# Kernel tuning notes

Measured on AMD Instinct MI355X. Metric: run time of the kernel, lower is better.

## Reference

```python
import jax, jax.numpy as jnp
import numpy as np

B, L, H, V = 64, 2048, 512, 34
T = 600           # max_decode_length hard-coded in Speller.forward
SOS_TOKEN = 0


def setup_inputs() -> dict:
    key = jax.random.key(0)
    ks = jax.random.split(key, 16)
    s = 1.0 / np.sqrt(H)
    p = lambda k, shape: (jax.random.uniform(k, shape, jnp.float32) * 2 - 1) * s
    return {
        "seq_embeddings": jax.random.normal(ks[0], (B, L, H), jnp.float32),
        "seq_lengths": jnp.maximum(jax.random.randint(ks[1], (B,), 0, L + 1), 1),
        "E_char": jax.random.normal(ks[2], (V, H), jnp.float32),      # nn.Embedding
        "W_key": p(ks[3], (H, H)), "b_key": p(ks[4], (H,)),           # Attention key_mlp
        "W_val": p(ks[5], (H, H)), "b_val": p(ks[6], (H,)),           # Attention value_mlp
        "W_ih": p(ks[7], (4 * H, 2 * H)), "W_hh": p(ks[8], (4 * H, H)),  # LSTMCell
        "b_ih": p(ks[9], (4 * H,)), "b_hh": p(ks[10], (4 * H,)),
        "W_cdn": p(ks[11], (V, 2 * H)), "b_cdn": p(ks[12], (V,)),     # cdn linear
    }


def reference(seq_embeddings, seq_lengths, E_char, W_key, b_key, W_val, b_val,
              W_ih, W_hh, b_ih, b_hh, W_cdn, b_cdn):
    Bz, Lz, Hz = seq_embeddings.shape
    # keys/values are time-invariant; compute once (same math as per-step recompute)
    keys = jnp.einsum('blh,kh->blk', seq_embeddings, W_key) + b_key       # (B,L,H)
    values = jnp.einsum('blh,kh->blk', seq_embeddings, W_val) + b_val     # (B,L,H)
    mask = jnp.arange(Lz)[None, :] < seq_lengths[:, None]                 # (B,L) ragged
    scale = 1.0 / jnp.sqrt(jnp.asarray(Hz, seq_embeddings.dtype))

    def attend(q):  # q: (B,H) -> masked softmax attention context (B,H)
        scores = jnp.einsum('blk,bk->bl', keys, q) * scale
        scores = jnp.where(mask, scores, -jnp.inf)
        w = jax.nn.softmax(scores, axis=1)                                # zeros past length
        return jnp.einsum('bl,blk->bk', w, values)

    h0 = jnp.zeros((Bz, Hz), seq_embeddings.dtype)
    c0 = jnp.zeros_like(h0)
    ctx0 = attend(h0)  # initial context with zero query -> uniform over valid positions
    rng = jax.random.key(42)

    def step(carry, t):
        prev_y, h, c, ctx = carry
        x = jnp.concatenate([E_char[prev_y], ctx], axis=1)                # (B,2H)
        gates = x @ W_ih.T + b_ih + h @ W_hh.T + b_hh                     # (B,4H)
        i, f, g, o = jnp.split(gates, 4, axis=1)
        c = jax.nn.sigmoid(f) * c + jax.nn.sigmoid(i) * jnp.tanh(g)
        h = jax.nn.sigmoid(o) * jnp.tanh(c)
        ctx = attend(h)
        logits = jnp.concatenate([h, ctx], axis=1) @ W_cdn.T + b_cdn      # (B,V)
        y = jax.random.categorical(jax.random.fold_in(rng, t), logits, axis=-1)
        return (y, h, c, ctx), y

    prev_y0 = jnp.full((Bz,), SOS_TOKEN, jnp.int32)
    _, ys = jax.lax.scan(step, (prev_y0, h0, c0, ctx0), jnp.arange(T))
    return ys.T  # (B, T) sampled symbols
```

## Files before the change

kernel.cpp:

```cpp
#include <hip/hip_runtime.h>
#include <cstdint>
#include <cfloat>
#include <cmath>

#define NB 64
#define LL 2048
#define HH 512
#define VV 34
#define TT 600
#define BLKT 512
#define GRID 256
#define GBLK 32
#define BSTRIDE 544

#define PARTITIONABLE 1

#define LDC(p)    __hip_atomic_load((p), __ATOMIC_RELAXED, __HIP_MEMORY_SCOPE_AGENT)
#define STC(p,v)  __hip_atomic_store((p), (v), __ATOMIC_RELAXED, __HIP_MEMORY_SCOPE_AGENT)

__device__ __forceinline__ float sigm_(float x){ return 1.0f/(1.0f+expf(-x)); }
__device__ __forceinline__ unsigned rotl_(unsigned x, int r){ return (x<<r)|(x>>(32-r)); }

__device__ __forceinline__ void tf2x32_(unsigned k0, unsigned k1, unsigned x0, unsigned x1,
                                        unsigned &o0, unsigned &o1){
  unsigned ks2 = k0 ^ k1 ^ 0x1BD11BDAu;
  x0 += k0; x1 += k1;
  x0+=x1; x1=rotl_(x1,13); x1^=x0;
  x0+=x1; x1=rotl_(x1,15); x1^=x0;
  x0+=x1; x1=rotl_(x1,26); x1^=x0;
  x0+=x1; x1=rotl_(x1, 6); x1^=x0;
  x0+=k1; x1+=ks2+1u;
  x0+=x1; x1=rotl_(x1,17); x1^=x0;
  x0+=x1; x1=rotl_(x1,29); x1^=x0;
  x0+=x1; x1=rotl_(x1,16); x1^=x0;
  x0+=x1; x1=rotl_(x1,24); x1^=x0;
  x0+=ks2; x1+=k0+2u;
  x0+=x1; x1=rotl_(x1,13); x1^=x0;
  x0+=x1; x1=rotl_(x1,15); x1^=x0;
  x0+=x1; x1=rotl_(x1,26); x1^=x0;
  x0+=x1; x1=rotl_(x1, 6); x1^=x0;
  x0+=k0; x1+=k1+3u;
  x0+=x1; x1=rotl_(x1,17); x1^=x0;
  x0+=x1; x1=rotl_(x1,29); x1^=x0;
  x0+=x1; x1=rotl_(x1,16); x1^=x0;
  x0+=x1; x1=rotl_(x1,24); x1^=x0;
  x0+=k1; x1+=ks2+4u;
  x0+=x1; x1=rotl_(x1,13); x1^=x0;
  x0+=x1; x1=rotl_(x1,15); x1^=x0;
  x0+=x1; x1=rotl_(x1,26); x1^=x0;
  x0+=x1; x1=rotl_(x1, 6); x1^=x0;
  x0+=ks2; x1+=k0+5u;
  o0 = x0; o1 = x1;
}

__device__ __forceinline__ void gumbel_emit_(int tid, int bb, int t, float* sZ,
                                             int* yv, int* out){
  if (tid < 34){
    unsigned kk0, kk1; tf2x32_(0u, 42u, 0u, (unsigned)t, kk0, kk1);
    int idx = bb*34 + tid;
    unsigned o0, o1, bits;
#if PARTITIONABLE
    tf2x32_(kk0, kk1, 0u, (unsigned)idx, o0, o1);
    bits = o0 ^ o1;
#else
    if (idx < 1088){ tf2x32_(kk0, kk1, (unsigned)idx, (unsigned)(idx+1088), o0, o1); bits = o0; }
    else           { tf2x32_(kk0, kk1, (unsigned)(idx-1088), (unsigned)idx, o0, o1); bits = o1; }
#endif
    float f = __uint_as_float((bits>>9) | 0x3f800000u) - 1.0f;
    float u = fmaxf(f, 1.17549435e-38f);
    sZ[tid] += -logf(-logf(u));
  }
  __syncthreads();
  if (tid == 0){
    float best = sZ[0]; int bi = 0;
    for (int v2=1; v2<34; v2++){ if (sZ[v2] > best){ best = sZ[v2]; bi = v2; } }
    STC(&yv[bb], bi);
    STC(&out[bb*TT + t], bi);
  }
}

__global__ __launch_bounds__(BLKT, 2) void speller_kernel_g32(
    const float* __restrict__ seq, const int* __restrict__ slen,
    const float* __restrict__ Ech, const float* __restrict__ Wkey,
    const float* __restrict__ Wval, const float* __restrict__ bval,
    const float* __restrict__ Wih, const float* __restrict__ Whh,
    const float* __restrict__ bih, const float* __restrict__ bhh,
    const float* __restrict__ Wcdn, const float* __restrict__ bcdn,
    int* __restrict__ out, float* __restrict__ ws, int MS, int CH)
{
  const int tid = threadIdx.x;
  const int bid = blockIdx.x;
  const int grp = bid & 7;
  const int li  = bid >> 3;

  float* h0   = ws;
  float* h1   = h0 + NB*HH;
  float* qt   = h1 + NB*HH;
  float* ctx  = qt + NB*HH;
  float* pm   = ctx + NB*HH;
  float* ps   = pm + NB*MS;
  float* pacc = ps + NB*MS;
  int*   iw   = (int*)(pacc + (size_t)NB*MS*HH);
  int*   yv   = iw;
  int*   bar  = iw + 64;

  __shared__ float sX[24*516];
  __shared__ float sRed[8*8*64];
  __shared__ float sGate[512];
  __shared__ float sAcc[8*512];
  __shared__ float sQt[512];
  __shared__ float sHb[512];
  __shared__ float sWm[8], sWs[8], sWf[8];
  __shared__ float sEb[512], sHs[512], sCt[512];
  __shared__ float sP[34*8];
  __shared__ float sZ[34];
  __shared__ float sAm[32], sAs[32], sAf[32];
  __shared__ float sSc[2];
  __shared__ int   sYv[8], sLen[8], sPref[9], sMap[8];

  float creg = 0.f;
  int epoch = 0;

  auto gbar = [&](){
    __syncthreads();
    epoch++;
    if (tid == 0)
      STC(&bar[grp*BSTRIDE + li*16], epoch);
    if (li == 0){
      if (tid < 32){
        while (LDC(&bar[grp*BSTRIDE + tid*16]) < epoch)
          __builtin_amdgcn_s_sleep(1);
      }
      if (tid == 0)
        STC(&bar[grp*BSTRIDE + 512], epoch);
    } else {
      if (tid == 0){
        while (LDC(&bar[grp*BSTRIDE + 512]) < epoch)
          __builtin_amdgcn_s_sleep(1);
      }
    }
    __syncthreads();
  };

  if (tid == 0){
    int ln[64]; unsigned char used[64];
    int load[8], cnt[8];
    for (int i=0;i<64;i++){
      int l = slen[i]; if (l<1) l=1; if (l>LL) l=LL;
      ln[i] = l; used[i] = 0;
    }
    for (int g2=0; g2<8; g2++){ load[g2]=0; cnt[g2]=0; }
    for (int it=0; it<64; it++){
      int bi = -1, bl = -1;
      for (int i=0;i<64;i++) if (!used[i] && ln[i] > bl){ bl = ln[i]; bi = i; }
      used[bi] = 1;
      int gi = -1, gl = 0x7fffffff;
      for (int g2=0; g2<8; g2++) if (cnt[g2] < 8 && load[g2] < gl){ gl = load[g2]; gi = g2; }
      if (gi == grp) sMap[cnt[gi]] = bi;
      load[gi] += bl; cnt[gi]++;
    }
  }
  __syncthreads();

  if (li < 8){
    int bb = sMap[li];
    STC(&h0[(size_t)bb*HH + tid], 0.f);
    STC(&h1[(size_t)bb*HH + tid], 0.f);
    STC(&qt[(size_t)bb*HH + tid], 0.f);
  }
  if (li == 8 && tid < 8) STC(&yv[sMap[tid]], 0);


  auto phaseA = [&](const float* hr, float* hw){
    if (tid < 8) sYv[tid] = LDC(&yv[sMap[tid]]);
    __syncthreads();
    #pragma unroll
    for (int i = 0; i < 24; i++){
      int b = i & 7, s = i >> 3;
      int bb = sMap[b];
      float v;
      if (s == 0)      v = Ech[(size_t)sYv[b]*HH + tid];
      else if (s == 1) v = LDC(&ctx[(size_t)bb*HH + tid]);
      else             v = LDC(&hr[(size_t)bb*HH + tid]);
      sX[i*516 + tid] = v;
    }
    __syncthreads();
    const int w = tid >> 6, lane = tid & 63, rr = lane >> 3, bb = lane & 7;
    float acc[8];
    #pragma unroll
    for (int o=0;o<8;o++) acc[o]=0.f;
    for (int kt = 0; kt < 12; kt++){
      const int sec = (kt < 4) ? 0 : (kt < 8) ? 1 : 2;
      const int cb4 = (kt & 3) * 128;
      #pragma unroll
      for (int it = 0; it < 4; it++){
        int kkb = w*16 + it*4;
        const float* xp = &sX[(sec*8 + bb)*516 + cb4 + kkb];
        float x0 = xp[0], x1 = xp[1], x2 = xp[2], x3 = xp[3];
        #pragma unroll
        for (int o = 0; o < 8; o++){
          int jl = o*8 + rr;
          int j  = (jl >> 4)*512 + li*16 + (jl & 15);
          const float* wp = (kt < 8) ? Wih + (size_t)j*1024 + kt*128 + kkb
                                     : Whh + (size_t)j*512  + (kt-8)*128 + kkb;
          float4 wv = *(const float4*)wp;
          acc[o] += wv.x*x0; acc[o] += wv.y*x1;
          acc[o] += wv.z*x2; acc[o] += wv.w*x3;
        }
      }
    }
    __syncthreads();
    #pragma unroll
    for (int o=0;o<8;o++) sRed[(w*8+o)*64 + lane] = acc[o];
    __syncthreads();
    {
      int jl = tid >> 3, b2 = tid & 7;
      int o = jl >> 3, rr2 = jl & 7;
      int j = (jl >> 4)*512 + li*16 + (jl & 15);
      float g = bih[j] + bhh[j];
      #pragma unroll
      for (int w2 = 0; w2 < 8; w2++) g += sRed[(w2*8+o)*64 + rr2*8 + b2];
      sGate[jl*8 + b2] = g;
    }
    __syncthreads();
    if (tid < 128){
      int kp = tid >> 3, b3 = tid & 7;
      float gi = sGate[(0*16+kp)*8 + b3];
      float gf = sGate[(1*16+kp)*8 + b3];
      float gg = sGate[(2*16+kp)*8 + b3];
      float go = sGate[(3*16+kp)*8 + b3];
      float cn = sigm_(gf)*creg + sigm_(gi)*tanhf(gg);
      creg = cn;
      STC(&hw[(size_t)sMap[b3]*HH + li*16 + kp], sigm_(go)*tanhf(cn));
    }
  };

  auto phaseB = [&](const float* hw){
    const int cc = li & 7;
    const int bp = li >> 3;
    const int bb0 = sMap[2*bp], bb1 = sMap[2*bp+1];
    sHb[tid] = LDC(&hw[(size_t)bb0*HH + tid]);
    sQt[tid] = LDC(&hw[(size_t)bb1*HH + tid]);
    float a = 0.f;
    const int c  = tid & 63;
    const int bs = (tid >> 6) & 1;
    for (int tile = 0; tile < 4; tile++){
      const int k0 = tile * 128;
      __syncthreads();
      {
        const float4* src = (const float4*)(Wkey + (size_t)k0*HH + cc*64);
        float4* dst = (float4*)sX;
        #pragma unroll
        for (int r = 0; r < 4; r++){
          int idx = r*512 + tid;
          int kk = idx >> 4, c4 = idx & 15;
          dst[kk*16 + c4] = src[(size_t)kk*(HH/4) + c4];
        }
      }
      __syncthreads();
      if (tid < 128){
        const float* hv = bs ? sQt : sHb;
        for (int kk = 0; kk < 128; kk++)
          a += sX[kk*64 + c] * hv[k0 + kk];
      }
    }
    __syncthreads();
    if (tid < 128){
      int bbX = bs ? bb1 : bb0;
      STC(&qt[(size_t)bbX*HH + cc*64 + c], a);
    }
  };

  auto phaseC = [&](){
    if (tid < 8){ int l = slen[sMap[tid]]; if(l<1)l=1; if(l>LL)l=LL; sLen[tid]=l; }
    __syncthreads();
    if (tid == 0){
      sPref[0] = 0;
      for (int i=0;i<8;i++) sPref[i+1] = sPref[i] + (sLen[i]+CH-1)/CH;
    }
    __syncthreads();
    const int gTot = sPref[8];
    const int w = tid >> 6, lane = tid & 63;
    const float SCALE = 1.0f / sqrtf(512.0f);
    const int start = (li*gTot)/GBLK, end = ((li+1)*gTot)/GBLK;
    int b = 0, bLast = -1;
    for (int c = start; c < end; ++c){
      while (sPref[b+1] <= c) b++;
      int slot = c - sPref[b];
      int l0 = slot * CH;
      int lend = min(l0 + CH, sLen[b]);
      int bb = sMap[b];
      if (b != bLast){
        __syncthreads();
        sQt[tid] = LDC(&qt[(size_t)bb*HH + tid]);
        bLast = b;
      }
      __syncthreads();
      const float4* qp = (const float4*)sQt;
      float4 qa = qp[lane], qb = qp[64+lane];
      float m = -FLT_MAX, ss = 0.f;
      float4 aA = make_float4(0,0,0,0), aB = make_float4(0,0,0,0);
      for (int ls = l0; ls < lend; ls += 64){
        float4 ra[8], rb[8];
        #pragma unroll
        for (int d=0; d<8; d++){
          int row = ls + w + d*8;
          if (row < lend){
            const float4* rp = (const float4*)(seq + ((size_t)bb*LL + row)*HH);
            ra[d] = rp[lane]; rb[d] = rp[64+lane];
          }
        }
        #pragma unroll
        for (int d=0; d<8; d++){
          int row = ls + w + d*8;
          if (row < lend){
            float4 ea = ra[d], eb = rb[d];
            float dd = ea.x*qa.x + ea.y*qa.y + ea.z*qa.z + ea.w*qa.w
                     + eb.x*qb.x + eb.y*qb.y + eb.z*qb.z + eb.w*qb.w;
            #pragma unroll
            for (int msk=1; msk<64; msk<<=1) dd += __shfl_xor(dd, msk, 64);
            float sc = dd * SCALE;
            float mn = fmaxf(m, sc);
            float r1 = expf(m - mn);
            float w1 = expf(sc - mn);
            ss = ss*r1 + w1;
            aA.x = aA.x*r1 + w1*ea.x; aA.y = aA.y*r1 + w1*ea.y;
            aA.z = aA.z*r1 + w1*ea.z; aA.w = aA.w*r1 + w1*ea.w;
            aB.x = aB.x*r1 + w1*eb.x; aB.y = aB.y*r1 + w1*eb.y;
            aB.z = aB.z*r1 + w1*eb.z; aB.w = aB.w*r1 + w1*eb.w;
            m = mn;
          }
        }
      }
      ((float4*)(sAcc + w*512))[lane]    = aA;
      ((float4*)(sAcc + w*512))[64+lane] = aB;
      if (lane == 0){ sWm[w] = m; sWs[w] = ss; }
      __syncthreads();
      if (tid == 0){
        float M = sWm[0];
        #pragma unroll
        for (int i=1;i<8;i++) M = fmaxf(M, sWm[i]);
        float S = 0.f;
        #pragma unroll
        for (int i=0;i<8;i++){ float f = expf(sWm[i]-M); sWf[i]=f; S += sWs[i]*f; }
        STC(&pm[bb*MS+slot], M); STC(&ps[bb*MS+slot], S);
      }
      __syncthreads();
      {
        float v = 0.f;
        #pragma unroll
        for (int i=0;i<8;i++) v += sAcc[i*512 + tid] * sWf[i];
        STC(&pacc[((size_t)(bb*MS+slot))*HH + tid], v);
      }
    }
  };

  auto phaseD = [&](int t, const float* hw){
    if (li < 8){
      const int bb = sMap[li];
      int ln = slen[bb]; if(ln<1)ln=1; if(ln>LL)ln=LL;
      const int nsl = (ln + CH - 1)/CH;
      if (tid < nsl){ sAm[tid] = LDC(&pm[bb*MS + tid]); sAs[tid] = LDC(&ps[bb*MS + tid]); }
      __syncthreads();
      if (tid == 0){
        float M = sAm[0];
        for (int s=1;s<nsl;s++) M = fmaxf(M, sAm[s]);
        float S = 0.f;
        for (int s=0;s<nsl;s++){ float f = expf(sAm[s]-M); sAf[s] = f; S += sAs[s]*f; }
        sSc[0] = S;
      }
      __syncthreads();
      {
        float S = sSc[0];
        float v = 0.f;
        #pragma unroll 8
        for (int s=0;s<nsl;s++) v += LDC(&pacc[((size_t)(bb*MS+s))*HH + tid]) * sAf[s];
        sEb[tid] = v / S;
        sHs[tid] = LDC(&hw[(size_t)bb*HH + tid]);
      }
      __syncthreads();
      {
        const float4* wr = (const float4*)(Wval + (size_t)tid*HH);
        const float4* er = (const float4*)sEb;
        float a = bval[tid];
        #pragma unroll 8
        for (int i=0;i<HH/4;i++){
          float4 w4 = wr[i], e4 = er[i];
          a += w4.x*e4.x; a += w4.y*e4.y; a += w4.z*e4.z; a += w4.w*e4.w;
        }
        sCt[tid] = a;
        STC(&ctx[(size_t)bb*HH + tid], a);
      }
      __syncthreads();
      if (t >= 0){
        if (tid < 34*8){
          int v = tid >> 3, ks = tid & 7;
          const float* wr = Wcdn + (size_t)v*1024 + ks*128;
          const float* xr = (ks < 4) ? (sHs + ks*128) : (sCt + (ks-4)*128);
          float p = 0.f;
          #pragma unroll 8
          for (int i=0;i<128;i++) p += wr[i]*xr[i];
          sP[v*8+ks] = p;
        }
        __syncthreads();
        if (tid < 34){
          float lg = bcdn[tid];
          #pragma unroll
          for (int i=0;i<8;i++) lg += sP[tid*8+i];
          sZ[tid] = lg;
        }
        __syncthreads();
        gumbel_emit_(tid, bb, t, sZ, yv, out);
      }
    }
  };

  gbar();
  phaseC();
  gbar();
  phaseD(-1, h0);
  gbar();
  for (int t = 0; t < TT; t++){
    const float* hr = (t & 1) ? h1 : h0;
    float* hwv      = (t & 1) ? h0 : h1;
    phaseA(hr, hwv);
    gbar();
    phaseB(hwv);
    gbar();
    phaseC();
    gbar();
    phaseD(t, hwv);
    gbar();
  }
}

extern "C" void kernel_launch(void* const* d_in, const int* in_sizes, int n_in,
                              void* d_out, int out_size, void* d_ws, size_t ws_size,
                              hipStream_t stream)
{
  const float* seq  = (const float*)d_in[0];
  const int*   slen = (const int*)d_in[1];
  const float* Ech  = (const float*)d_in[2];
  const float* Wkey = (const float*)d_in[3];
  const float* Wval = (const float*)d_in[5];
  const float* bval = (const float*)d_in[6];
  const float* Wih  = (const float*)d_in[7];
  const float* Whh  = (const float*)d_in[8];
  const float* bih  = (const float*)d_in[9];
  const float* bhh  = (const float*)d_in[10];
  const float* Wcdn = (const float*)d_in[11];
  const float* bcdn = (const float*)d_in[12];
  int*   out = (int*)d_out;
  float* ws  = (float*)d_ws;

  int MS = 32;
  size_t floats_total;
  while (true){
    floats_total = 4*(size_t)NB*HH + (size_t)NB*MS*(2 + HH);
    size_t need = (floats_total + 64 + 8*BSTRIDE + 64)*4;
    if (need <= ws_size || MS == 1) break;
    MS >>= 1;
  }
  int CH = 2048 / MS;

  size_t bar_off = (floats_total + 64)*4;
  hipMemsetAsync((char*)d_ws + bar_off, 0, 8*BSTRIDE*4, stream);

  void* args[] = { (void*)&seq, (void*)&slen, (void*)&Ech, (void*)&Wkey,
                   (void*)&Wval, (void*)&bval, (void*)&Wih, (void*)&Whh,
                   (void*)&bih, (void*)&bhh, (void*)&Wcdn, (void*)&bcdn,
                   (void*)&out, (void*)&ws, (void*)&MS, (void*)&CH };

  hipLaunchCooperativeKernel((void*)speller_kernel_g32, dim3(GRID), dim3(BLKT),
                             args, 0, stream);
}
```

Measured before the change: 71.00 ms.

## Split context phase across all group blocks and flatten group barrier

The per-batch context phase, previously run by only 8 of 32 blocks per group, is split into three phases. These are the softmax-combine, the Wval projection and the logits/sampling step, and the first two are spread over all 32 blocks by column quarters, reusing the stale h buffer as scratch for the normalized context. The group barrier is also flattened so every block polls all 32 block flags directly instead of going through a leader block. This trades more parallelism per phase for two extra grid barriers per decode step and more polling traffic.

```diff
diff --git a/kernel.cpp b/kernel.cpp
--- a/kernel.cpp
+++ b/kernel.cpp
@@ -126,18 +126,9 @@
     epoch++;
     if (tid == 0)
       STC(&bar[grp*BSTRIDE + li*16], epoch);
-    if (li == 0){
-      if (tid < 32){
-        while (LDC(&bar[grp*BSTRIDE + tid*16]) < epoch)
-          __builtin_amdgcn_s_sleep(1);
-      }
-      if (tid == 0)
-        STC(&bar[grp*BSTRIDE + 512], epoch);
-    } else {
-      if (tid == 0){
-        while (LDC(&bar[grp*BSTRIDE + 512]) < epoch)
-          __builtin_amdgcn_s_sleep(1);
-      }
+    if (tid < 32){
+      while (LDC(&bar[grp*BSTRIDE + tid*16]) < epoch)
+        __builtin_amdgcn_s_sleep(1);
     }
     __syncthreads();
   };
@@ -355,70 +346,83 @@
     }
   };
 
-  auto phaseD = [&](int t, const float* hw){
+  auto phaseD1 = [&](float* eb){
+    const int bq = li >> 2, qq = li & 3;
+    const int bb = sMap[bq];
+    int ln = slen[bb]; if(ln<1)ln=1; if(ln>LL)ln=LL;
+    const int nsl = (ln + CH - 1)/CH;
+    if (tid < nsl){ sAm[tid] = LDC(&pm[bb*MS + tid]); sAs[tid] = LDC(&ps[bb*MS + tid]); }
+    __syncthreads();
+    if (tid == 0){
+      float M = sAm[0];
+      for (int s=1;s<nsl;s++) M = fmaxf(M, sAm[s]);
+      float S = 0.f;
+      for (int s=0;s<nsl;s++){ float f = expf(sAm[s]-M); sAf[s] = f; S += sAs[s]*f; }
+      sSc[0] = S;
+    }
+    __syncthreads();
+    if (tid < 128){
+      const int col = qq*128 + tid;
+      const float S = sSc[0];
+      float v = 0.f;
+      #pragma unroll 8
+      for (int s=0;s<nsl;s++) v += LDC(&pacc[((size_t)(bb*MS+s))*HH + col]) * sAf[s];
+      STC(&eb[(size_t)bb*HH + col], v / S);
+    }
+  };
+
+  auto phaseD2 = [&](const float* eb){
+    const int bq = li >> 2, qq = li & 3;
+    const int bb = sMap[bq];
+    sEb[tid] = LDC(&eb[(size_t)bb*HH + tid]);
+    __syncthreads();
+    if (tid < 128){
+      const int col = qq*128 + tid;
+      const float4* wr = (const float4*)(Wval + (size_t)col*HH);
+      const float4* er = (const float4*)sEb;
+      float a = bval[col];
+      #pragma unroll 8
+      for (int i=0;i<HH/4;i++){
+        float4 w4 = wr[i], e4 = er[i];
+        a += w4.x*e4.x; a += w4.y*e4.y; a += w4.z*e4.z; a += w4.w*e4.w;
+      }
+      STC(&ctx[(size_t)bb*HH + col], a);
+    }
+  };
+
+  auto phaseD3 = [&](int t, const float* hw){
     if (li < 8){
       const int bb = sMap[li];
-      int ln = slen[bb]; if(ln<1)ln=1; if(ln>LL)ln=LL;
-      const int nsl = (ln + CH - 1)/CH;
-      if (tid < nsl){ sAm[tid] = LDC(&pm[bb*MS + tid]); sAs[tid] = LDC(&ps[bb*MS + tid]); }
-      __syncthreads();
-      if (tid == 0){
-        float M = sAm[0];
-        for (int s=1;s<nsl;s++) M = fmaxf(M, sAm[s]);
-        float S = 0.f;
-        for (int s=0;s<nsl;s++){ float f = expf(sAm[s]-M); sAf[s] = f; S += sAs[s]*f; }
-        sSc[0] = S;
-      }
-      __syncthreads();
-      {
-        float S = sSc[0];
-        float v = 0.f;
+      sHs[tid] = LDC(&hw[(size_t)bb*HH + tid]);
+      sCt[tid] = LDC(&ctx[(size_t)bb*HH + tid]);
+      __syncthreads();
+      if (tid < 34*8){
+        int v = tid >> 3, ks = tid & 7;
+        const float* wr = Wcdn + (size_t)v*1024 + ks*128;
+        const float* xr = (ks < 4) ? (sHs + ks*128) : (sCt + (ks-4)*128);
+        float p = 0.f;
         #pragma unroll 8
-        for (int s=0;s<nsl;s++) v += LDC(&pacc[((size_t)(bb*MS+s))*HH + tid]) * sAf[s];
-        sEb[tid] = v / S;
-        sHs[tid] = LDC(&hw[(size_t)bb*HH + tid]);
-      }
-      __syncthreads();
-      {
-        const float4* wr = (const float4*)(Wval + (size_t)tid*HH);
-        const float4* er = (const float4*)sEb;
-        float a = bval[tid];
-        #pragma unroll 8
-        for (int i=0;i<HH/4;i++){
-          float4 w4 = wr[i], e4 = er[i];
-          a += w4.x*e4.x; a += w4.y*e4.y; a += w4.z*e4.z; a += w4.w*e4.w;
-        }
-        sCt[tid] = a;
-        STC(&ctx[(size_t)bb*HH + tid], a);
-      }
-      __syncthreads();
-      if (t >= 0){
-        if (tid < 34*8){
-          int v = tid >> 3, ks = tid & 7;
-          const float* wr = Wcdn + (size_t)v*1024 + ks*128;
-          const float* xr = (ks < 4) ? (sHs + ks*128) : (sCt + (ks-4)*128);
-          float p = 0.f;
-          #pragma unroll 8
-          for (int i=0;i<128;i++) p += wr[i]*xr[i];
-          sP[v*8+ks] = p;
-        }
-        __syncthreads();
-        if (tid < 34){
-          float lg = bcdn[tid];
-          #pragma unroll
-          for (int i=0;i<8;i++) lg += sP[tid*8+i];
-          sZ[tid] = lg;
-        }
-        __syncthreads();
-        gumbel_emit_(tid, bb, t, sZ, yv, out);
-      }
+        for (int i=0;i<128;i++) p += wr[i]*xr[i];
+        sP[v*8+ks] = p;
+      }
+      __syncthreads();
+      if (tid < 34){
+        float lg = bcdn[tid];
+        #pragma unroll
+        for (int i=0;i<8;i++) lg += sP[tid*8+i];
+        sZ[tid] = lg;
+      }
+      __syncthreads();
+      gumbel_emit_(tid, bb, t, sZ, yv, out);
     }
   };
 
   gbar();
   phaseC();
   gbar();
-  phaseD(-1, h0);
+  phaseD1(h1);
+  gbar();
+  phaseD2(h1);
   gbar();
   for (int t = 0; t < TT; t++){
     const float* hr = (t & 1) ? h1 : h0;
@@ -429,7 +433,11 @@
     gbar();
     phaseC();
     gbar();
-    phaseD(t, hwv);
+    phaseD1((float*)hr);
+    gbar();
+    phaseD2(hr);
+    gbar();
+    phaseD3(t, hwv);
     gbar();
   }
 }
```

After: 62.01 ms. 1.14x faster.

## Split attention combine across all blocks, widen atomic loads, flatten group barrier

Applied to the files above, without the earlier changes.

Phase D's partial-softmax combine, previously run by only 8 blocks per group, is split out into a new phase D1. In D1 all 32 blocks each reduce a quarter of one batch row's context vector and write it to a scratch buffer, reusing the stale h buffer. This adds one extra group barrier per step. The barrier is changed so every block polls all 32 arrival flags directly instead of using a two-level leader relay. Cross-block loads and stores of h, ctx, qt and pacc now use 64-bit relaxed atomics to halve the number of memory operations.

```diff
diff --git a/kernel.cpp b/kernel.cpp
--- a/kernel.cpp
+++ b/kernel.cpp
@@ -12,6 +12,8 @@
 #define GRID 256
 #define GBLK 32
 #define BSTRIDE 544
+
+typedef unsigned long long u64;
 
 #define PARTITIONABLE 1
 
@@ -126,18 +128,9 @@
     epoch++;
     if (tid == 0)
       STC(&bar[grp*BSTRIDE + li*16], epoch);
-    if (li == 0){
-      if (tid < 32){
-        while (LDC(&bar[grp*BSTRIDE + tid*16]) < epoch)
-          __builtin_amdgcn_s_sleep(1);
-      }
-      if (tid == 0)
-        STC(&bar[grp*BSTRIDE + 512], epoch);
-    } else {
-      if (tid == 0){
-        while (LDC(&bar[grp*BSTRIDE + 512]) < epoch)
-          __builtin_amdgcn_s_sleep(1);
-      }
+    if (tid < 32){
+      while (LDC(&bar[grp*BSTRIDE + tid*16]) < epoch)
+        __builtin_amdgcn_s_sleep(1);
     }
     __syncthreads();
   };
@@ -175,14 +168,20 @@
     if (tid < 8) sYv[tid] = LDC(&yv[sMap[tid]]);
     __syncthreads();
     #pragma unroll
-    for (int i = 0; i < 24; i++){
-      int b = i & 7, s = i >> 3;
-      int bb = sMap[b];
-      float v;
-      if (s == 0)      v = Ech[(size_t)sYv[b]*HH + tid];
-      else if (s == 1) v = LDC(&ctx[(size_t)bb*HH + tid]);
-      else             v = LDC(&hr[(size_t)bb*HH + tid]);
-      sX[i*516 + tid] = v;
+    for (int i = 0; i < 8; i++)
+      sX[i*516 + tid] = Ech[(size_t)sYv[i]*HH + tid];
+    #pragma unroll
+    for (int ii = 0; ii < 8; ii++){
+      int idx = ii*512 + tid;
+      int r   = idx >> 8;
+      int c2  = (idx & 255) << 1;
+      int b   = r & 7, s = r >> 3;
+      int bb  = sMap[b];
+      const float* src = (s == 0 ? ctx : hr) + (size_t)bb*HH + c2;
+      u64 v = LDC((const u64*)src);
+      union { u64 u; float f[2]; } cv; cv.u = v;
+      sX[(8 + r)*516 + c2]     = cv.f[0];
+      sX[(8 + r)*516 + c2 + 1] = cv.f[1];
     }
     __syncthreads();
     const int w = tid >> 6, lane = tid & 63, rr = lane >> 3, bb = lane & 7;
@@ -239,8 +238,14 @@
     const int cc = li & 7;
     const int bp = li >> 3;
     const int bb0 = sMap[2*bp], bb1 = sMap[2*bp+1];
-    sHb[tid] = LDC(&hw[(size_t)bb0*HH + tid]);
-    sQt[tid] = LDC(&hw[(size_t)bb1*HH + tid]);
+    {
+      int t2 = tid & 255, which = tid >> 8;
+      const float* src = hw + (size_t)(which ? bb1 : bb0)*HH + t2*2;
+      u64 v = LDC((const u64*)src);
+      union { u64 u; float f[2]; } cv; cv.u = v;
+      float* dstv = which ? sQt : sHb;
+      dstv[t2*2] = cv.f[0]; dstv[t2*2+1] = cv.f[1];
+    }
     float a = 0.f;
     const int c  = tid & 63;
     const int bs = (tid >> 6) & 1;
@@ -292,7 +297,11 @@
       int bb = sMap[b];
       if (b != bLast){
         __syncthreads();
-        sQt[tid] = LDC(&qt[(size_t)bb*HH + tid]);
+        if (tid < 256){
+          u64 v = LDC((const u64*)(qt + (size_t)bb*HH + tid*2));
+          union { u64 u; float f[2]; } cv; cv.u = v;
+          sQt[tid*2] = cv.f[0]; sQt[tid*2+1] = cv.f[1];
+        }
         bLast = b;
       }
       __syncthreads();
@@ -346,37 +355,62 @@
         STC(&pm[bb*MS+slot], M); STC(&ps[bb*MS+slot], S);
       }
       __syncthreads();
-      {
-        float v = 0.f;
-        #pragma unroll
-        for (int i=0;i<8;i++) v += sAcc[i*512 + tid] * sWf[i];
-        STC(&pacc[((size_t)(bb*MS+slot))*HH + tid], v);
+      if (tid < 256){
+        float v0 = 0.f, v1 = 0.f;
+        #pragma unroll
+        for (int i=0;i<8;i++){
+          v0 += sAcc[i*512 + 2*tid]     * sWf[i];
+          v1 += sAcc[i*512 + 2*tid + 1] * sWf[i];
+        }
+        union { float f[2]; u64 u; } cv; cv.f[0] = v0; cv.f[1] = v1;
+        STC((u64*)&pacc[((size_t)(bb*MS+slot))*HH + 2*tid], cv.u);
       }
     }
   };
 
-  auto phaseD = [&](int t, const float* hw){
+  auto phaseD1 = [&](float* eb){
+    const int bq = li >> 2, qq = li & 3;
+    const int bb = sMap[bq];
+    int ln = slen[bb]; if(ln<1)ln=1; if(ln>LL)ln=LL;
+    const int nsl = (ln + CH - 1)/CH;
+    if (tid < nsl){ sAm[tid] = LDC(&pm[bb*MS + tid]); sAs[tid] = LDC(&ps[bb*MS + tid]); }
+    __syncthreads();
+    if (tid == 0){
+      float M = sAm[0];
+      for (int s=1;s<nsl;s++) M = fmaxf(M, sAm[s]);
+      float S = 0.f;
+      for (int s=0;s<nsl;s++){ float f = expf(sAm[s]-M); sAf[s] = f; S += sAs[s]*f; }
+      sSc[0] = S;
+    }
+    __syncthreads();
+    if (tid < 64){
+      const int col = qq*128 + tid*2;
+      const float S = sSc[0];
+      float v0 = 0.f, v1 = 0.f;
+      #pragma unroll 8
+      for (int s=0;s<nsl;s++){
+        u64 w = LDC((const u64*)&pacc[((size_t)(bb*MS+s))*HH + col]);
+        union { u64 u; float f[2]; } cv; cv.u = w;
+        v0 += cv.f[0] * sAf[s];
+        v1 += cv.f[1] * sAf[s];
+      }
+      union { float f[2]; u64 u; } ov; ov.f[0] = v0/S; ov.f[1] = v1/S;
+      STC((u64*)&eb[(size_t)bb*HH + col], ov.u);
+    }
+  };
+
+  auto phaseD23 = [&](int t, const float* eb, const float* hw){
     if (li < 8){
       const int bb = sMap[li];
-      int ln = slen[bb]; if(ln<1)ln=1; if(ln>LL)ln=LL;
-      const int nsl = (ln + CH - 1)/CH;
-      if (tid < nsl){ sAm[tid] = LDC(&pm[bb*MS + tid]); sAs[tid] = LDC(&ps[bb*MS + tid]); }
-      __syncthreads();
-      if (tid == 0){
-        float M = sAm[0];
-        for (int s=1;s<nsl;s++) M = fmaxf(M, sAm[s]);
-        float S = 0.f;
-        for (int s=0;s<nsl;s++){ float f = expf(sAm[s]-M); sAf[s] = f; S += sAs[s]*f; }
-        sSc[0] = S;
-      }
-      __syncthreads();
-      {
-        float S = sSc[0];
-        float v = 0.f;
-        #pragma unroll 8
-        for (int s=0;s<nsl;s++) v += LDC(&pacc[((size_t)(bb*MS+s))*HH + tid]) * sAf[s];
-        sEb[tid] = v / S;
-        sHs[tid] = LDC(&hw[(size_t)bb*HH + tid]);
+      if (tid < 256){
+        u64 v = LDC((const u64*)(eb + (size_t)bb*HH + tid*2));
+        union { u64 u; float f[2]; } cv; cv.u = v;
+        sEb[tid*2] = cv.f[0]; sEb[tid*2+1] = cv.f[1];
+      } else {
+        int t2 = tid - 256;
+        u64 v = LDC((const u64*)(hw + (size_t)bb*HH + t2*2));
+        union { u64 u; float f[2]; } cv; cv.u = v;
+        sHs[t2*2] = cv.f[0]; sHs[t2*2+1] = cv.f[1];
       }
       __syncthreads();
       {
@@ -389,9 +423,13 @@
           a += w4.x*e4.x; a += w4.y*e4.y; a += w4.z*e4.z; a += w4.w*e4.w;
         }
         sCt[tid] = a;
-        STC(&ctx[(size_t)bb*HH + tid], a);
-      }
-      __syncthreads();
+      }
+      __syncthreads();
+      if (tid < 256){
+        union { float f[2]; u64 u; } cv;
+        cv.f[0] = sCt[tid*2]; cv.f[1] = sCt[tid*2+1];
+        STC((u64*)&ctx[(size_t)bb*HH + tid*2], cv.u);
+      }
       if (t >= 0){
         if (tid < 34*8){
           int v = tid >> 3, ks = tid & 7;
@@ -418,7 +456,9 @@
   gbar();
   phaseC();
   gbar();
-  phaseD(-1, h0);
+  phaseD1(h1);
+  gbar();
+  phaseD23(-1, h1, h0);
   gbar();
   for (int t = 0; t < TT; t++){
     const float* hr = (t & 1) ? h1 : h0;
@@ -429,7 +469,9 @@
     gbar();
     phaseC();
     gbar();
-    phaseD(t, hwv);
+    phaseD1((float*)hr);
+    gbar();
+    phaseD23(t, hr, hwv);
     gbar();
   }
 }
```

After: 75.25 ms. 6.0% more time.
